# Kernel tuning notes

Measured on AMD Instinct MI355X. Metric: run time of the kernel, lower is better.

Reference implementation:

```python
import jax, jax.numpy as jnp
import numpy as np
from jax import lax

V, E, H, K = 100000, 256, 512, 12
B, T = 64, 256
START, END, PAD = 10, 11, 0
NEG = -100000.0


def setup_inputs() -> dict:
    key = jax.random.key(0)
    ks = jax.random.split(key, 16)
    Hd = H // 2
    def n(k, shape, s=0.1):
        return jax.random.normal(k, shape, jnp.float32) * s
    sentence = jax.random.randint(ks[0], (B, T), 0, V)
    sentence_chars = jnp.zeros((B, T, 16), jnp.int32)
    emb = jax.random.normal(ks[1], (V, E), jnp.float32)
    Wih_f, Whh_f = n(ks[2], (4 * Hd, E)), n(ks[3], (4 * Hd, Hd))
    bih_f, bhh_f = n(ks[4], (4 * Hd,)), n(ks[5], (4 * Hd,))
    Wih_b, Whh_b = n(ks[6], (4 * Hd, E)), n(ks[7], (4 * Hd, Hd))
    bih_b, bhh_b = n(ks[8], (4 * Hd,)), n(ks[9], (4 * Hd,))
    Wp, bp = n(ks[10], (K, H)), n(ks[11], (K,))
    # transitions[i, j] = score of transitioning from tag j to tag i
    trans = jax.random.normal(ks[12], (K, K), jnp.float32)
    trans = trans.at[START, :].set(NEG)
    trans = trans.at[:, END].set(NEG)
    trans = trans.at[:, PAD].set(NEG)
    trans = trans.at[PAD, :].set(NEG)
    trans = trans.at[PAD, PAD].set(0.0)
    trans = trans.at[PAD, END].set(0.0)
    h0 = jax.random.normal(ks[13], (2, B, Hd), jnp.float32)
    c0 = jax.random.normal(ks[14], (2, B, Hd), jnp.float32)
    return dict(sentence=sentence, sentence_chars=sentence_chars, emb=emb,
                Wih_f=Wih_f, Whh_f=Whh_f, bih_f=bih_f, bhh_f=bhh_f,
                Wih_b=Wih_b, Whh_b=Whh_b, bih_b=bih_b, bhh_b=bhh_b,
                Wp=Wp, bp=bp, transitions=trans, h0=h0, c0=c0)


def _lstm_dir(x, Wih, Whh, bih, bhh, h, c, reverse):
    # x: [B, T, E] -> hs: [B, T, Hd]; PyTorch LSTM gate order i,f,g,o
    def step(carry, xt):
        h, c = carry
        g = xt @ Wih.T + bih + h @ Whh.T + bhh
        i, f, gg, o = jnp.split(g, 4, axis=-1)
        c = jax.nn.sigmoid(f) * c + jax.nn.sigmoid(i) * jnp.tanh(gg)
        h = jax.nn.sigmoid(o) * jnp.tanh(c)
        return (h, c), h
    _, hs = lax.scan(step, (h, c), jnp.swapaxes(x, 0, 1), reverse=reverse)
    return jnp.swapaxes(hs, 0, 1)


def _viterbi(features, transitions, lengths):
    b, t, k = features.shape
    score0 = jnp.full((b, k), -10000.0, features.dtype).at[:, START].set(0.0)
    def step(score, feat_t):
        m = score[:, None, :] + transitions[None]  # [B, K(to), K(from)]
        bptr = jnp.argmax(m, axis=-1)              # [B, K]
        new = jnp.max(m, axis=-1) + feat_t
        return new, bptr
    final, bptrs = lax.scan(step, score0, jnp.swapaxes(features, 0, 1))  # bptrs [T,B,K]
    best_score = jnp.max(final, axis=-1)
    best_tag = jnp.argmax(final, axis=-1)
    ts = jnp.arange(t)
    def backtrack(x, inp):
        tt, bp = inp  # bp: [B, K]
        emit = x      # p_t (valid where tt < length)
        nxt = jnp.take_along_axis(bp, x[:, None], axis=1)[:, 0]
        x = jnp.where(tt < lengths, nxt, x)
        return x, emit
    _, ps = lax.scan(backtrack, best_tag, (ts, bptrs), reverse=True)  # [T, B]
    paths = jnp.swapaxes(ps, 0, 1)
    paths = jnp.where(jnp.arange(t)[None, :] < lengths[:, None], paths, -1)
    return paths, best_score


def reference(sentence, sentence_chars, emb, Wih_f, Whh_f, bih_f, bhh_f,
              Wih_b, Whh_b, bih_b, bhh_b, Wp, bp, transitions, h0, c0):
    mask = sentence > 0
    lengths = mask.sum(axis=1)
    x = emb[sentence]  # [B, T, E]
    hf = _lstm_dir(x, Wih_f, Whh_f, bih_f, bhh_f, h0[0], c0[0], False)
    hb = _lstm_dir(x, Wih_b, Whh_b, bih_b, bhh_b, h0[1], c0[1], True)
    feats = jnp.concatenate([hf, hb], axis=-1) @ Wp.T + bp  # [B, T, K]
    paths, best_score = _viterbi(feats, transitions, lengths)
    return paths, best_score
```

## Files before the change

kernel.cpp:

```cpp
#include <hip/hip_runtime.h>


#define NB 64
#define NT 256
#define NKTAG 12
#define START_TAG 10
#define KK_SLAB2 18
#define KK_REG2 46

typedef unsigned short u16;
typedef _Float16 half2v __attribute__((ext_vector_type(2)));
typedef _Float16 half8 __attribute__((ext_vector_type(8)));
typedef float f32x4 __attribute__((ext_vector_type(4)));

__device__ __forceinline__ float b2f(u16 u) {
  union { unsigned int i; float f; } v; v.i = ((unsigned int)u) << 16; return v.f;
}
__device__ __forceinline__ u16 f2b(float f) {
  union { float f; unsigned int i; } v; v.f = f;
  unsigned int r = v.i + 0x7FFFu + ((v.i >> 16) & 1u);
  return (u16)(r >> 16);
}
__device__ __forceinline__ u16 f2h(float f) {
  union { _Float16 h; u16 u; } v; v.h = (_Float16)f; return v.u;
}
__device__ __forceinline__ unsigned int pkh(float x, float y) {
  return (unsigned int)f2h(x) | ((unsigned int)f2h(y) << 16);
}
__device__ __forceinline__ float fsig(float x) { return 1.0f / (1.0f + __expf(-x)); }
__device__ __forceinline__ float ftanh(float x) { return 2.0f / (1.0f + __expf(-2.0f * x)) - 1.0f; }

__device__ __forceinline__ float dot2h(unsigned int a, unsigned int b, float c) {
#if __has_builtin(__builtin_amdgcn_fdot2)
  union { unsigned int u; half2v h; } va, vb;
  va.u = a; vb.u = b;
  return __builtin_amdgcn_fdot2(va.h, vb.h, c, false);
#else
  float d;
  asm("v_dot2_f32_f16 %0, %1, %2, %3" : "=v"(d) : "v"(a), "v"(b), "v"(c));
  return d;
#endif
}

__global__ __launch_bounds__(256) void pack_whh(const float* __restrict__ Whf,
                                                const float* __restrict__ Whb,
                                                const float* __restrict__ Wp,
                                                uint4* __restrict__ WT,
                                                unsigned int* __restrict__ WpH) {
  if (blockIdx.x == 256) {
    for (int it = 0; it < 12; ++it) {
      int idx = it * 256 + threadIdx.x;
      int k = idx >> 8, cc = idx & 255;
      WpH[idx] = pkh(Wp[(size_t)k * 512 + 2 * cc], Wp[(size_t)k * 512 + 2 * cc + 1]);
    }
    return;
  }
  int gid = blockIdx.x * 256 + threadIdx.x;
  int d = gid >> 15;
  int rem = gid & 32767;
  int kk = rem >> 8, j = rem & 255;
  const float* W = d ? Whb : Whf;
  int k0 = kk * 2;
  uint4 o;
  o.x = pkh(W[(size_t)j * 256 + k0],         W[(size_t)j * 256 + k0 + 1]);
  o.y = pkh(W[(size_t)(j + 256) * 256 + k0], W[(size_t)(j + 256) * 256 + k0 + 1]);
  o.z = pkh(W[(size_t)(j + 512) * 256 + k0], W[(size_t)(j + 512) * 256 + k0 + 1]);
  o.w = pkh(W[(size_t)(j + 768) * 256 + k0], W[(size_t)(j + 768) * 256 + k0 + 1]);
  WT[gid] = o;
}

__global__ __launch_bounds__(256) void gemm_x(const int* __restrict__ sent,
                                              const float* __restrict__ emb,
                                              const float* __restrict__ Wf,
                                              const float* __restrict__ Wb,
                                              const float* __restrict__ bihf,
                                              const float* __restrict__ bhhf,
                                              const float* __restrict__ bihb,
                                              const float* __restrict__ bhhb,
                                              u16* __restrict__ X4) {
  __shared__ _Float16 A_lds[128][40];
  __shared__ _Float16 B_lds[64][40];
  __shared__ int tok[128];
  __shared__ u16 Xs[128][80];
  int tid = threadIdx.x;
  int lin = blockIdx.y * 32 + blockIdx.x;
  int swz = (lin & 7) * 512 + (lin >> 3);
  int in = swz & 31;
  int im = swz >> 5;
  int d = in >> 4, j0 = (in & 15) * 16;
  if (tid < 128) tok[tid] = sent[im * 128 + tid];

  int w = tid >> 6, l = tid & 63;
  int lrow = l & 15, lk = l >> 4;
  f32x4 acc[2][4];
#pragma unroll
  for (int mt = 0; mt < 2; ++mt)
#pragma unroll
    for (int nt = 0; nt < 4; ++nt) acc[mt][nt] = (f32x4)0.0f;

  int arow = tid >> 1, akh = tid & 1;
  int brow = tid & 63, bkq = tid >> 6;
  int r_w = ((brow >> 4) << 8) + j0 + (brow & 15);
  const float* wrow = (d ? Wb : Wf) + (size_t)r_w * 256;

  for (int kc = 0; kc < 8; ++kc) {
    int k0 = kc * 32;
    __syncthreads();
    {
      const float* ap = emb + (size_t)tok[arow] * 256 + k0 + akh * 16;
#pragma unroll
      for (int q = 0; q < 2; ++q) {
        float4 v0 = *(const float4*)(ap + q * 8);
        float4 v1 = *(const float4*)(ap + q * 8 + 4);
        uint4 pk;
        pk.x = pkh(v0.x, v0.y); pk.y = pkh(v0.z, v0.w);
        pk.z = pkh(v1.x, v1.y); pk.w = pkh(v1.z, v1.w);
        *(uint4*)&A_lds[arow][akh * 16 + q * 8] = pk;
      }
    }
    {
      float4 v0 = *(const float4*)(wrow + k0 + bkq * 8);
      float4 v1 = *(const float4*)(wrow + k0 + bkq * 8 + 4);
      uint4 pk;
      pk.x = pkh(v0.x, v0.y); pk.y = pkh(v0.z, v0.w);
      pk.z = pkh(v1.x, v1.y); pk.w = pkh(v1.z, v1.w);
      *(uint4*)&B_lds[brow][bkq * 8] = pk;
    }
    __syncthreads();
    half8 af[2], bf[4];
#pragma unroll
    for (int mt = 0; mt < 2; ++mt)
      af[mt] = *(const half8*)&A_lds[w * 32 + mt * 16 + lrow][lk * 8];
#pragma unroll
    for (int nt = 0; nt < 4; ++nt)
      bf[nt] = *(const half8*)&B_lds[nt * 16 + lrow][lk * 8];
#pragma unroll
    for (int mt = 0; mt < 2; ++mt)
#pragma unroll
      for (int nt = 0; nt < 4; ++nt)
        acc[mt][nt] = __builtin_amdgcn_mfma_f32_16x16x32_f16(af[mt], bf[nt], acc[mt][nt], 0, 0, 0);
  }
  float bias[4];
#pragma unroll
  for (int nt = 0; nt < 4; ++nt) {
    int rr = nt * 256 + j0 + lrow;
    bias[nt] = d ? (bihb[rr] + bhhb[rr]) : (bihf[rr] + bhhf[rr]);
  }
  __syncthreads();
#pragma unroll
  for (int mt = 0; mt < 2; ++mt)
#pragma unroll
    for (int r = 0; r < 4; ++r) {
      int row = w * 32 + mt * 16 + lk * 4 + r;
      uint2 pk;
      pk.x = (unsigned int)f2b(acc[mt][0][r] + bias[0]) |
             ((unsigned int)f2b(acc[mt][1][r] + bias[1]) << 16);
      pk.y = (unsigned int)f2b(acc[mt][2][r] + bias[2]) |
             ((unsigned int)f2b(acc[mt][3][r] + bias[3]) << 16);
      *(uint2*)&Xs[row][lrow * 4] = pk;
    }
  __syncthreads();
  int frow = tid >> 1, fh = tid & 1;
  int i = im * 128 + frow;
  int bb = i >> 8, tt = i & 255;
  size_t base = (((size_t)d * NT + tt) * NB + bb) * 1024 + (size_t)j0 * 4 + fh * 32;
#pragma unroll
  for (int q = 0; q < 4; ++q)
    *(uint4*)&X4[base + q * 8] = *(const uint4*)&Xs[frow][fh * 32 + q * 8];
}

__global__ __launch_bounds__(512, 2) void lstm_scan(const uint4* __restrict__ WT,
                                                    const ushort4* __restrict__ X4,
                                                    const float* __restrict__ h0,
                                                    const float* __restrict__ c0,
                                                    u16* __restrict__ H) {
  int d = blockIdx.x >> 6, b = blockIdx.x & 63;
  int tid = threadIdx.x;
  int jj = tid & 255, g = tid >> 8;
  __shared__ uint4 wlds[2 * KK_SLAB2 * 256];
  __shared__ uint4 h2s4[32];
  __shared__ float4 plds[256];
  const uint4* Ws = WT + (size_t)d * 32768;
  for (int e = tid; e < 2 * KK_SLAB2 * 256; e += 512) {
    int sr = e >> 8, j2 = e & 255;
    int gg = sr / KK_SLAB2, r = sr - gg * KK_SLAB2;
    wlds[e] = Ws[(size_t)(gg * 64 + r) * 256 + j2];
  }
  uint4 wreg[KK_REG2];
#pragma unroll
  for (int r = 0; r < KK_REG2; ++r)
    wreg[r] = Ws[(size_t)(g * 64 + KK_SLAB2 + r) * 256 + jj];
  float c = 0.f;
  if (g == 0) c = c0[((size_t)d * NB + b) * 256 + jj];
  if (tid < 256) ((u16*)h2s4)[tid] = f2h(h0[((size_t)d * NB + b) * 256 + tid]);
  __syncthreads();
  for (int s = 0; s < NT; ++s) {
    int t = d ? (NT - 1 - s) : s;
    ushort4 xg = make_ushort4(0, 0, 0, 0);
    if (g == 0) xg = X4[(((size_t)d * NT + t) * NB + b) * 256 + jj];
    float ai = 0.f, af = 0.f, ag = 0.f, ao = 0.f;
#pragma unroll
    for (int q = 0; q < 16; ++q) {
      uint4 h4 = h2s4[g * 16 + q];
      unsigned int hp[4] = {h4.x, h4.y, h4.z, h4.w};
#pragma unroll
      for (int e = 0; e < 4; ++e) {
        int kkl = q * 4 + e;
        uint4 wv;
        if (kkl < KK_SLAB2) wv = wlds[((g * KK_SLAB2 + kkl) << 8) | jj];
        else                wv = wreg[kkl - KK_SLAB2];
        ai = dot2h(wv.x, hp[e], ai); af = dot2h(wv.y, hp[e], af);
        ag = dot2h(wv.z, hp[e], ag); ao = dot2h(wv.w, hp[e], ao);
      }
    }
    if (g) plds[jj] = make_float4(ai, af, ag, ao);
    __syncthreads();
    if (g == 0) {
      float4 p0 = plds[jj];
      ai += p0.x + b2f(xg.x);
      af += p0.y + b2f(xg.y);
      ag += p0.z + b2f(xg.z);
      ao += p0.w + b2f(xg.w);
      float ii = fsig(ai), ff = fsig(af), gg2 = ftanh(ag), oo = fsig(ao);
      c = ff * c + ii * gg2;
      float h = oo * ftanh(c);
      u16 hu = f2h(h);
      ((u16*)h2s4)[jj] = hu;
      H[(((size_t)d * NB + b) * NT + t) * 256 + jj] = hu;
    }
    __syncthreads();
  }
}

__global__ __launch_bounds__(384) void feats_kernel(const u16* __restrict__ H,
                                                    const unsigned int* __restrict__ WpH,
                                                    const float* __restrict__ bp,
                                                    float* __restrict__ FT) {
  __shared__ uint4 hbuf[32][65];
  __shared__ uint4 wbuf[64][12];
  int tid = threadIdx.x;
  int i0 = blockIdx.x * 32;
  for (int idx = tid; idx < 768; idx += 384) {
    int it = idx / 12, k = idx - it * 12;
    wbuf[it][k] = ((const uint4*)WpH)[k * 64 + it];
  }
  for (int idx = tid; idx < 2048; idx += 384) {
    int row = idx >> 6, c4 = idx & 63;
    int i = i0 + row;
    int b = i >> 8, t = i & 255;
    int dd = c4 >> 5, cc = c4 & 31;
    const uint4* hpg = (const uint4*)(H + (((size_t)dd * NB + b) * NT + t) * 256);
    hbuf[row][c4] = hpg[cc];
  }
  __syncthreads();
  int row = tid / 12, k = tid - row * 12;
  float s0 = 0.f, s1 = 0.f, s2 = 0.f, s3 = 0.f;
#pragma unroll 8
  for (int it = 0; it < 64; ++it) {
    uint4 h4 = hbuf[row][it];
    uint4 w4 = wbuf[it][k];
    s0 = dot2h(h4.x, w4.x, s0); s1 = dot2h(h4.y, w4.y, s1);
    s2 = dot2h(h4.z, w4.z, s2); s3 = dot2h(h4.w, w4.w, s3);
  }
  int i = i0 + row;
  FT[(size_t)i * NKTAG + k] = (s0 + s1) + (s2 + s3) + bp[k];
}

__global__ __launch_bounds__(64) void viterbi_kernel(const float* __restrict__ FT,
                                                     const float* __restrict__ trans,
                                                     const int* __restrict__ sent,
                                                     float* __restrict__ out) {
  int b = blockIdx.x, tid = threadIdx.x;
  __shared__ float trans_s[12][12];
  __shared__ float s_s[12];
  __shared__ unsigned char bp_s[256][12];
  __shared__ int path_s[256];
  for (int idx = tid; idx < 144; idx += 64) trans_s[idx / 12][idx % 12] = trans[idx];
  int cnt = 0;
#pragma unroll
  for (int q = 0; q < 4; ++q) cnt += (sent[b * NT + q * 64 + tid] > 0) ? 1 : 0;
  for (int off = 32; off; off >>= 1) cnt += __shfl_down(cnt, off);
  int len = __shfl(cnt, 0);
  if (tid < 12) s_s[tid] = (tid == START_TAG) ? 0.f : -10000.f;
  float f_next = (tid < 12) ? FT[((size_t)b * NT) * NKTAG + tid] : 0.f;
  __syncthreads();
  for (int t = 0; t < NT; ++t) {
    float best = 0.f, f = f_next;
    int barg = 0;
    if (t + 1 < NT && tid < 12)
      f_next = FT[((size_t)b * NT + t + 1) * NKTAG + tid];
    if (tid < 12) {
      best = s_s[0] + trans_s[tid][0];
      barg = 0;
#pragma unroll
      for (int fr = 1; fr < 12; ++fr) {
        float v = s_s[fr] + trans_s[tid][fr];
        if (v > best) { best = v; barg = fr; }
      }
    }
    __syncthreads();
    if (tid < 12) {
      s_s[tid] = best + f;
      bp_s[t][tid] = (unsigned char)barg;
    }
    __syncthreads();
  }
  if (tid == 0) {
    float bs = s_s[0];
    int bt = 0;
    for (int k = 1; k < 12; ++k)
      if (s_s[k] > bs) { bs = s_s[k]; bt = k; }
    out[NB * NT + b] = bs;
    int x = bt;
    for (int tt = NT - 1; tt >= 0; --tt) {
      path_s[tt] = x;
      int nxt = bp_s[tt][x];
      if (tt < len) x = nxt;
    }
  }
  __syncthreads();
#pragma unroll
  for (int q = 0; q < 4; ++q) {
    int t = q * 64 + tid;
    out[b * NT + t] = (t < len) ? (float)path_s[t] : -1.0f;
  }
}

extern "C" void kernel_launch(void* const* d_in, const int* in_sizes, int n_in,
                              void* d_out, int out_size, void* d_ws, size_t ws_size,
                              hipStream_t stream) {
  (void)in_sizes; (void)n_in; (void)out_size; (void)ws_size;
  const int*   sent  = (const int*)d_in[0];
  const float* emb   = (const float*)d_in[2];
  const float* Wih_f = (const float*)d_in[3];
  const float* Whh_f = (const float*)d_in[4];
  const float* bih_f = (const float*)d_in[5];
  const float* bhh_f = (const float*)d_in[6];
  const float* Wih_b = (const float*)d_in[7];
  const float* Whh_b = (const float*)d_in[8];
  const float* bih_b = (const float*)d_in[9];
  const float* bhh_b = (const float*)d_in[10];
  const float* Wp    = (const float*)d_in[11];
  const float* bp    = (const float*)d_in[12];
  const float* trans = (const float*)d_in[13];
  const float* h0    = (const float*)d_in[14];
  const float* c0    = (const float*)d_in[15];
  float* out = (float*)d_out;

  char* w = (char*)d_ws;
  u16*   X4  = (u16*)w;
  uint4* WTH = (uint4*)(w + 67108864);
  float* FT  = (float*)(w + 68157440);
  unsigned int* WpH = (unsigned int*)(w + 68943872);
  u16*   H   = (u16*)(w + 68956160);

  pack_whh<<<dim3(257), dim3(256), 0, stream>>>(Whh_f, Whh_b, Wp, WTH, WpH);
  gemm_x<<<dim3(32, 128), dim3(256), 0, stream>>>(sent, emb, Wih_f, Wih_b,
                                                  bih_f, bhh_f, bih_b, bhh_b, X4);
  lstm_scan<<<dim3(128), dim3(512), 0, stream>>>(WTH, (const ushort4*)X4, h0, c0, H);
  feats_kernel<<<dim3(512), dim3(384), 0, stream>>>(H, WpH, bp, FT);
  viterbi_kernel<<<dim3(64), dim3(64), 0, stream>>>(FT, trans, sent, out);
}
```

Baseline: 566.5 us.

## Run LSTM scan with one thread per hidden unit and double-buffered h

```diff
diff --git a/kernel.cpp b/kernel.cpp
--- a/kernel.cpp
+++ b/kernel.cpp
@@ -5,8 +5,8 @@
 #define NT 256
 #define NKTAG 12
 #define START_TAG 10
-#define KK_SLAB2 18
-#define KK_REG2 46
+#define KK_SLAB3 32
+#define KK_REG3 96
 
 typedef unsigned short u16;
 typedef _Float16 half2v __attribute__((ext_vector_type(2)));
@@ -169,65 +169,50 @@
     *(uint4*)&X4[base + q * 8] = *(const uint4*)&Xs[frow][fh * 32 + q * 8];
 }
 
-__global__ __launch_bounds__(512, 2) void lstm_scan(const uint4* __restrict__ WT,
+__global__ __launch_bounds__(256, 1) void lstm_scan(const uint4* __restrict__ WT,
                                                     const ushort4* __restrict__ X4,
                                                     const float* __restrict__ h0,
                                                     const float* __restrict__ c0,
                                                     u16* __restrict__ H) {
   int d = blockIdx.x >> 6, b = blockIdx.x & 63;
-  int tid = threadIdx.x;
-  int jj = tid & 255, g = tid >> 8;
-  __shared__ uint4 wlds[2 * KK_SLAB2 * 256];
-  __shared__ uint4 h2s4[32];
-  __shared__ float4 plds[256];
+  int jj = threadIdx.x;
+  __shared__ uint4 wlds[KK_SLAB3 * 256];
+  __shared__ uint4 hbuf2[2][32];
   const uint4* Ws = WT + (size_t)d * 32768;
-  for (int e = tid; e < 2 * KK_SLAB2 * 256; e += 512) {
-    int sr = e >> 8, j2 = e & 255;
-    int gg = sr / KK_SLAB2, r = sr - gg * KK_SLAB2;
-    wlds[e] = Ws[(size_t)(gg * 64 + r) * 256 + j2];
-  }
-  uint4 wreg[KK_REG2];
-#pragma unroll
-  for (int r = 0; r < KK_REG2; ++r)
-    wreg[r] = Ws[(size_t)(g * 64 + KK_SLAB2 + r) * 256 + jj];
-  float c = 0.f;
-  if (g == 0) c = c0[((size_t)d * NB + b) * 256 + jj];
-  if (tid < 256) ((u16*)h2s4)[tid] = f2h(h0[((size_t)d * NB + b) * 256 + tid]);
+  for (int e = jj; e < KK_SLAB3 * 256; e += 256) wlds[e] = Ws[e];
+  uint4 wreg[KK_REG3];
+#pragma unroll
+  for (int r = 0; r < KK_REG3; ++r)
+    wreg[r] = Ws[(size_t)(KK_SLAB3 + r) * 256 + jj];
+  float c = c0[((size_t)d * NB + b) * 256 + jj];
+  ((u16*)hbuf2[0])[jj] = f2h(h0[((size_t)d * NB + b) * 256 + jj]);
   __syncthreads();
   for (int s = 0; s < NT; ++s) {
     int t = d ? (NT - 1 - s) : s;
-    ushort4 xg = make_ushort4(0, 0, 0, 0);
-    if (g == 0) xg = X4[(((size_t)d * NT + t) * NB + b) * 256 + jj];
+    ushort4 xg = X4[(((size_t)d * NT + t) * NB + b) * 256 + jj];
+    const uint4* hb = hbuf2[s & 1];
     float ai = 0.f, af = 0.f, ag = 0.f, ao = 0.f;
 #pragma unroll
-    for (int q = 0; q < 16; ++q) {
-      uint4 h4 = h2s4[g * 16 + q];
+    for (int q = 0; q < 32; ++q) {
+      uint4 h4 = hb[q];
       unsigned int hp[4] = {h4.x, h4.y, h4.z, h4.w};
 #pragma unroll
       for (int e = 0; e < 4; ++e) {
-        int kkl = q * 4 + e;
+        int kk = q * 4 + e;
         uint4 wv;
-        if (kkl < KK_SLAB2) wv = wlds[((g * KK_SLAB2 + kkl) << 8) | jj];
-        else                wv = wreg[kkl - KK_SLAB2];
+        if (kk < KK_SLAB3) wv = wlds[(kk << 8) | jj];
+        else               wv = wreg[kk - KK_SLAB3];
         ai = dot2h(wv.x, hp[e], ai); af = dot2h(wv.y, hp[e], af);
         ag = dot2h(wv.z, hp[e], ag); ao = dot2h(wv.w, hp[e], ao);
       }
     }
-    if (g) plds[jj] = make_float4(ai, af, ag, ao);
-    __syncthreads();
-    if (g == 0) {
-      float4 p0 = plds[jj];
-      ai += p0.x + b2f(xg.x);
-      af += p0.y + b2f(xg.y);
-      ag += p0.z + b2f(xg.z);
-      ao += p0.w + b2f(xg.w);
-      float ii = fsig(ai), ff = fsig(af), gg2 = ftanh(ag), oo = fsig(ao);
-      c = ff * c + ii * gg2;
-      float h = oo * ftanh(c);
-      u16 hu = f2h(h);
-      ((u16*)h2s4)[jj] = hu;
-      H[(((size_t)d * NB + b) * NT + t) * 256 + jj] = hu;
-    }
+    ai += b2f(xg.x); af += b2f(xg.y); ag += b2f(xg.z); ao += b2f(xg.w);
+    float ii = fsig(ai), ff = fsig(af), gg = ftanh(ag), oo = fsig(ao);
+    c = ff * c + ii * gg;
+    float h = oo * ftanh(c);
+    u16 hu = f2h(h);
+    ((u16*)hbuf2[(s + 1) & 1])[jj] = hu;
+    H[(((size_t)d * NB + b) * NT + t) * 256 + jj] = hu;
     __syncthreads();
   }
 }
@@ -357,7 +342,7 @@
   pack_whh<<<dim3(257), dim3(256), 0, stream>>>(Whh_f, Whh_b, Wp, WTH, WpH);
   gemm_x<<<dim3(32, 128), dim3(256), 0, stream>>>(sent, emb, Wih_f, Wih_b,
                                                   bih_f, bhh_f, bih_b, bhh_b, X4);
-  lstm_scan<<<dim3(128), dim3(512), 0, stream>>>(WTH, (const ushort4*)X4, h0, c0, H);
+  lstm_scan<<<dim3(128), dim3(256), 0, stream>>>(WTH, (const ushort4*)X4, h0, c0, H);
   feats_kernel<<<dim3(512), dim3(384), 0, stream>>>(H, WpH, bp, FT);
   viterbi_kernel<<<dim3(64), dim3(64), 0, stream>>>(FT, trans, sent, out);
 }
```

Result: slower. 1.064 ms (+87.8%).
